# Optimization experiments

Measured on AMD Instinct MI355X. Metric: run time of the kernel, lower is better.

Reference implementation:

```python
import jax, jax.numpy as jnp
import numpy as np
import math

B, L, D, H = 4, 2048, 1024, 16
HD = D // H


def setup_inputs() -> dict:
    key = jax.random.key(0)
    k1, k2, k3 = jax.random.split(key, 3)
    x = jax.random.normal(k1, (B, L, D), dtype=jnp.float32)
    # Linear weights stored as [in, out] so y = x @ W (equivalent to torch x @ W.T)
    Wqkv = jax.random.normal(k2, (D, 3 * D), dtype=jnp.float32) * (1.0 / math.sqrt(D))
    Wproj = jax.random.normal(k3, (D, D), dtype=jnp.float32) * (1.0 / math.sqrt(D))
    attn_mask = jnp.tril(jnp.ones((L, L), dtype=bool))  # True = attend (causal)
    key_padding_mask = jnp.zeros((B, L), dtype=bool)     # True = padded (none here)
    return {"x": x, "Wqkv": Wqkv, "Wproj": Wproj,
            "attn_mask": attn_mask, "key_padding_mask": key_padding_mask}


def reference(x, Wqkv, Wproj, attn_mask, key_padding_mask):
    Bx, Lx, Dx = x.shape
    qkv = x @ Wqkv                              # [B, L, 3D]
    q, k, v = jnp.split(qkv, 3, axis=-1)
    def shape(t):
        return t.reshape(Bx, Lx, H, HD).transpose(0, 2, 1, 3)  # [B, H, L, hd]
    q, k, v = shape(q), shape(k), shape(v)
    att = jnp.einsum('bhqd,bhkd->bhqk', q, k) / math.sqrt(HD)  # [B, H, L, L]
    neg_inf = jnp.float32(-jnp.inf)
    att = jnp.where(attn_mask[None, None, :, :], att, neg_inf)
    att = jnp.where(key_padding_mask[:, None, None, :], neg_inf, att)
    att = jax.nn.softmax(att, axis=-1)
    y = jnp.einsum('bhqk,bhkd->bhqd', att, v)   # [B, H, L, hd]
    y = y.transpose(0, 2, 1, 3).reshape(Bx, Lx, Dx)
    return y @ Wproj
```

## Files before the change

### kernel.cpp

```cpp
#include <hip/hip_runtime.h>
#include <cstdint>
#include <cstddef>


typedef __attribute__((ext_vector_type(8))) __bf16 bf16x8;
typedef __attribute__((ext_vector_type(4))) __bf16 bf16x4;
typedef __attribute__((ext_vector_type(4))) float f32x4;

__device__ __forceinline__ f32x4 mfma_bf16(bf16x8 a, bf16x8 b, f32x4 c) {
  return __builtin_amdgcn_mfma_f32_16x16x32_bf16(a, b, c, 0, 0, 0);
}

__device__ __forceinline__ void async_copy16(const void* gsrc, void* ldsdst) {
  __builtin_amdgcn_global_load_lds(
      (const __attribute__((address_space(1))) void*)gsrc,
      (__attribute__((address_space(3))) void*)ldsdst, 16, 0, 0);
}

__global__ __launch_bounds__(256) void f32_to_bf16(
    const float* __restrict__ in, __bf16* __restrict__ out) {
  const size_t i = ((size_t)blockIdx.x * 256 + threadIdx.x) * 4;
  const float4 v = *(const float4*)&in[i];
  bf16x4 o = {(__bf16)v.x, (__bf16)v.y, (__bf16)v.z, (__bf16)v.w};
  *(bf16x4*)&out[i] = o;
}

__global__ __launch_bounds__(256) void transpose_f32_bf16(
    const float* __restrict__ in, __bf16* __restrict__ out, int R, int C) {
  __shared__ float tile[32][33];
  const int c0 = blockIdx.x * 32;
  const int r0 = blockIdx.y * 32;
  const int tx = threadIdx.x & 31;
  const int ty = threadIdx.x >> 5;
#pragma unroll
  for (int i = 0; i < 32; i += 8)
    tile[ty + i][tx] = in[(size_t)(r0 + ty + i) * C + c0 + tx];
  __syncthreads();
#pragma unroll
  for (int i = 0; i < 32; i += 8)
    out[(size_t)(c0 + ty + i) * R + r0 + tx] = (__bf16)tile[tx][ty + i];
}


__global__ __launch_bounds__(256) void gemm_bt_f32out(
    const __bf16* __restrict__ A, const __bf16* __restrict__ BT,
    float* __restrict__ C, int M, int N, int K) {
  __shared__ __bf16 As[128 * 32];
  __shared__ __bf16 Bs[128 * 32];
  const int tid = threadIdx.x;
  const int wave = tid >> 6;
  const int lane = tid & 63;
  const int n16 = lane & 15;
  const int quad = lane >> 4;
  const int m0 = blockIdx.x * 128;
  const int n0 = blockIdx.y * 128;
  const int wr = wave >> 1;
  const int wc = wave & 1;

  const f32x4 zero = {0.f, 0.f, 0.f, 0.f};
  f32x4 acc[4][4];
#pragma unroll
  for (int i = 0; i < 4; ++i)
#pragma unroll
    for (int j = 0; j < 4; ++j) acc[i][j] = zero;

  const int KT = K >> 5;
  for (int kt = 0; kt < KT; ++kt) {
    const int k0 = kt << 5;
#pragma unroll
    for (int r = 0; r < 2; ++r) {
      const int li = (r << 8) + tid;
      const int row = li >> 2;
      const int kp8 = (li & 3) << 3;
      const int lbase = ((r << 8) + (wave << 6)) << 3;
      async_copy16(&A[(size_t)(m0 + row) * K + k0 + kp8], &As[lbase]);
      async_copy16(&BT[(size_t)(n0 + row) * K + k0 + kp8], &Bs[lbase]);
    }
    __syncthreads();
    bf16x8 af[4], bf[4];
#pragma unroll
    for (int t = 0; t < 4; ++t) {
      af[t] = *(const bf16x8*)&As[(wr * 64 + t * 16 + n16) * 32 + quad * 8];
      bf[t] = *(const bf16x8*)&Bs[(wc * 64 + t * 16 + n16) * 32 + quad * 8];
    }
#pragma unroll
    for (int mt = 0; mt < 4; ++mt)
#pragma unroll
      for (int nt = 0; nt < 4; ++nt)
        acc[mt][nt] = mfma_bf16(af[mt], bf[nt], acc[mt][nt]);
    __syncthreads();
  }
#pragma unroll
  for (int mt = 0; mt < 4; ++mt) {
#pragma unroll
    for (int r = 0; r < 4; ++r) {
      const int m = m0 + wr * 64 + mt * 16 + quad * 4 + r;
#pragma unroll
      for (int nt = 0; nt < 4; ++nt) {
        const int n = n0 + wc * 64 + nt * 16 + n16;
        C[(size_t)m * N + n] = acc[mt][nt][r];
      }
    }
  }
}

__global__ __launch_bounds__(256) void gemm_qkv(
    const __bf16* __restrict__ A, const __bf16* __restrict__ BT,
    __bf16* __restrict__ Q, __bf16* __restrict__ Kh, __bf16* __restrict__ VT) {
  __shared__ __bf16 As[128 * 32];
  __shared__ __bf16 Bs[128 * 32];
  const int tid = threadIdx.x;
  const int wave = tid >> 6;
  const int lane = tid & 63;
  const int n16 = lane & 15;
  const int quad = lane >> 4;
  const int m0 = blockIdx.x * 128;
  const int n0 = blockIdx.y * 128;
  const int wr = wave >> 1;
  const int wc = wave & 1;
  const int K = 1024;

  const f32x4 zero = {0.f, 0.f, 0.f, 0.f};
  f32x4 acc[4][4];
#pragma unroll
  for (int i = 0; i < 4; ++i)
#pragma unroll
    for (int j = 0; j < 4; ++j) acc[i][j] = zero;

  for (int kt = 0; kt < 32; ++kt) {
    const int k0 = kt << 5;
#pragma unroll
    for (int r = 0; r < 2; ++r) {
      const int li = (r << 8) + tid;
      const int row = li >> 2;
      const int kp8 = (li & 3) << 3;
      const int lbase = ((r << 8) + (wave << 6)) << 3;
      async_copy16(&A[(size_t)(m0 + row) * K + k0 + kp8], &As[lbase]);
      async_copy16(&BT[(size_t)(n0 + row) * K + k0 + kp8], &Bs[lbase]);
    }
    __syncthreads();
    bf16x8 af[4], bf[4];
#pragma unroll
    for (int t = 0; t < 4; ++t) {
      af[t] = *(const bf16x8*)&As[(wr * 64 + t * 16 + n16) * 32 + quad * 8];
      bf[t] = *(const bf16x8*)&Bs[(wc * 64 + t * 16 + n16) * 32 + quad * 8];
    }
#pragma unroll
    for (int mt = 0; mt < 4; ++mt)
#pragma unroll
      for (int nt = 0; nt < 4; ++nt)
        acc[mt][nt] = mfma_bf16(af[mt], bf[nt], acc[mt][nt]);
    __syncthreads();
  }

  __syncthreads();
  const int b = m0 >> 11;
  __bf16* tw = (wave < 2 ? As : Bs) + (wave & 1) * 2048;
  const int l0w = (m0 & 2047) + wr * 64;

  if (n0 < 2048) {
    const float QSCALE = 0.125f * 1.44269504089f;
    const bool isQ = (n0 < 1024);
    const int h = ((n0 & 1023) >> 6) + wc;
    __bf16* dst = isQ ? Q : Kh;
    const size_t base = ((size_t)(b * 16 + h) * 2048) * 64;
#pragma unroll
    for (int pass = 0; pass < 2; ++pass) {
#pragma unroll
      for (int mt = 2 * pass; mt < 2 * pass + 2; ++mt) {
#pragma unroll
        for (int nt = 0; nt < 4; ++nt)
#pragma unroll
          for (int r = 0; r < 4; ++r) {
            const int hd = nt * 16 + n16;
            const int mm = (mt & 1) * 16 + quad * 4 + r;
            const float v =
                isQ ? acc[mt][nt][r] * QSCALE : acc[mt][nt][r];
            tw[mm * 64 + (((hd >> 3) ^ (mm & 7)) << 3) + (hd & 7)] =
                (__bf16)v;
          }
      }
#pragma unroll
      for (int i = 0; i < 4; ++i) {
        const int c = lane + 64 * i;
        const int row = c >> 3;
        const int hd0 = (c & 7) << 3;
        const int phys = (c & 7) ^ (row & 7);
        const bf16x8 v = *(const bf16x8*)&tw[row * 64 + phys * 8];
        *(bf16x8*)&dst[base + (size_t)(l0w + pass * 32 + row) * 64 + hd0] = v;
      }
    }
  } else {
    const int h = ((n0 - 2048) >> 6) + wc;
    const size_t bhead = (size_t)(b * 16 + h);
#pragma unroll
    for (int pass = 0; pass < 2; ++pass) {
#pragma unroll
      for (int nt = 2 * pass; nt < 2 * pass + 2; ++nt) {
#pragma unroll
        for (int mt = 0; mt < 4; ++mt)
#pragma unroll
          for (int r = 0; r < 4; ++r) {
            const int hdp = (nt & 1) * 16 + n16;
            const int mm = mt * 16 + quad * 4 + r;
            const int phys = (mm >> 3) ^ (hdp & 7);
            tw[hdp * 64 + phys * 8 + (mm & 7)] = (__bf16)acc[mt][nt][r];
          }
      }
#pragma unroll
      for (int i = 0; i < 4; ++i) {
        const int c = lane + 64 * i;
        const int row = c >> 3;
        const int phys = (c & 7) ^ (row & 7);
        const bf16x8 v = *(const bf16x8*)&tw[row * 64 + phys * 8];
        *(bf16x8*)&VT[(bhead * 64 + pass * 32 + row) * 2048 + l0w +
                      (c & 7) * 8] = v;
      }
    }
  }
}

__global__ __launch_bounds__(256, 4) void flash_attn(
    const __bf16* __restrict__ Q, const __bf16* __restrict__ Kh,
    const __bf16* __restrict__ VT, __bf16* __restrict__ Y) {
  __shared__ __bf16 KsB[2][32 * 64];
  __shared__ __bf16 VsB[2][64 * 32];
  __shared__ __bf16 Ps[4][16 * 40];
  const int bh = blockIdx.x;
  const int p = blockIdx.y;
  const int tid = threadIdx.x;
  const int wave = tid >> 6;
  const int lane = tid & 63;
  const int n16 = lane & 15;
  const int quad = lane >> 4;
  __bf16* pb = Ps[wave];
  const __bf16* Qb = Q + (size_t)bh * 2048 * 64;
  const __bf16* Kb = Kh + (size_t)bh * 2048 * 64;
  const __bf16* Vb = VT + (size_t)bh * 64 * 2048;
  const int b = bh >> 4;
  const int h = bh & 15;
  const f32x4 zero = {0.f, 0.f, 0.f, 0.f};

  const int krow = wave * 8 + (lane >> 3);
  const int kcol8 = (((lane & 7) ^ (lane >> 3)) << 3);
  const int vrow = wave * 16 + (lane >> 2);
  const int vcol8 = (((lane & 3) ^ quad) << 3);

#pragma unroll
  for (int t = 0; t < 2; ++t) {
    const int qt = t == 0 ? p : 31 - p;
    const int q0w = qt * 64 + wave * 16;

    bf16x8 qf[2];
#pragma unroll
    for (int kh = 0; kh < 2; ++kh)
      qf[kh] = *(const bf16x8*)&Qb[(size_t)(q0w + n16) * 64 + kh * 32 +
                                   quad * 8];

    f32x4 o[4];
#pragma unroll
    for (int j = 0; j < 4; ++j) o[j] = zero;
    float lsum = 0.f;

    const int nsteps = 2 * qt + 2;

    async_copy16(&Kb[(size_t)krow * 64 + kcol8], &KsB[0][wave * 512]);
    async_copy16(&Vb[(size_t)vrow * 2048 + vcol8], &VsB[0][wave * 512]);

    for (int kt = 0; kt < nsteps; ++kt) {
      const int buf = kt & 1;
      const int c0 = kt * 32;
      __syncthreads();
      if (kt + 1 < nsteps) {
        const int nb = buf ^ 1;
        const int cn = c0 + 32;
        async_copy16(&Kb[(size_t)(cn + krow) * 64 + kcol8],
                     &KsB[nb][wave * 512]);
        async_copy16(&Vb[(size_t)vrow * 2048 + cn + vcol8],
                     &VsB[nb][wave * 512]);
      }
      const __bf16* ks = KsB[buf];
      const __bf16* vs = VsB[buf];

      f32x4 s[2];
      s[0] = zero;
      s[1] = zero;
#pragma unroll
      for (int ct = 0; ct < 2; ++ct) {
#pragma unroll
        for (int kh = 0; kh < 2; ++kh) {
          const bf16x8 kf = *(const bf16x8*)&ks[(ct * 16 + n16) * 64 +
                                                (((kh * 4 + quad) ^ (n16 & 7))
                                                 << 3)];
          s[ct] = mfma_bf16(kf, qf[kh], s[ct]);
        }
      }
      if (kt >= 2 * qt) {
        const int myq = q0w + n16;
#pragma unroll
        for (int ct = 0; ct < 2; ++ct)
#pragma unroll
          for (int r = 0; r < 4; ++r) {
            const int kcol = c0 + ct * 16 + quad * 4 + r;
            float e = __builtin_amdgcn_exp2f(s[ct][r]);
            e = (kcol <= myq) ? e : 0.f;
            s[ct][r] = e;
            lsum += e;
          }
      } else {
#pragma unroll
        for (int ct = 0; ct < 2; ++ct)
#pragma unroll
          for (int r = 0; r < 4; ++r) {
            const float e = __builtin_amdgcn_exp2f(s[ct][r]);
            s[ct][r] = e;
            lsum += e;
          }
      }
#pragma unroll
      for (int ct = 0; ct < 2; ++ct) {
        const bf16x4 pk = {(__bf16)s[ct][0], (__bf16)s[ct][1],
                           (__bf16)s[ct][2], (__bf16)s[ct][3]};
        *(bf16x4*)&pb[n16 * 40 + ct * 16 + quad * 4] = pk;
      }
      const bf16x8 pa = *(const bf16x8*)&pb[n16 * 40 + quad * 8];
#pragma unroll
      for (int ht = 0; ht < 4; ++ht) {
        const bf16x8 vf = *(const bf16x8*)&vs[(ht * 16 + n16) * 32 +
                                              ((quad ^ (n16 >> 2)) << 3)];
        o[ht] = mfma_bf16(pa, vf, o[ht]);
      }
    }

    lsum += __shfl_xor(lsum, 16);
    lsum += __shfl_xor(lsum, 32);
    const float inv = 1.0f / lsum;
#pragma unroll
    for (int r = 0; r < 4; ++r) {
      const float invr = __shfl(inv, quad * 4 + r);
      const int row = q0w + quad * 4 + r;
#pragma unroll
      for (int ht = 0; ht < 4; ++ht)
        Y[(size_t)(b * 2048 + row) * 1024 + h * 64 + ht * 16 + n16] =
            (__bf16)(o[ht][r] * invr);
    }
  }
}

extern "C" void kernel_launch(void* const* d_in, const int* in_sizes, int n_in,
                              void* d_out, int out_size, void* d_ws,
                              size_t ws_size, hipStream_t stream) {
  const float* x = (const float*)d_in[0];
  const float* Wqkv = (const float*)d_in[1];
  const float* Wproj = (const float*)d_in[2];
  float* out = (float*)d_out;

  char* ws = (char*)d_ws;
  __bf16* xb = (__bf16*)ws;     ws += (size_t)8192 * 1024 * 2;
  __bf16* WqkvT = (__bf16*)ws;  ws += (size_t)3072 * 1024 * 2;
  __bf16* WprojT = (__bf16*)ws; ws += (size_t)1024 * 1024 * 2;
  __bf16* Qs = (__bf16*)ws;     ws += (size_t)64 * 2048 * 64 * 2;
  __bf16* Ks = (__bf16*)ws;     ws += (size_t)64 * 2048 * 64 * 2;
  __bf16* VTs = (__bf16*)ws;    ws += (size_t)64 * 64 * 2048 * 2;
  __bf16* attn = xb;

  f32_to_bf16<<<8192, 256, 0, stream>>>(x, xb);
  transpose_f32_bf16<<<dim3(96, 32), 256, 0, stream>>>(Wqkv, WqkvT, 1024, 3072);
  transpose_f32_bf16<<<dim3(32, 32), 256, 0, stream>>>(Wproj, WprojT, 1024, 1024);
  gemm_qkv<<<dim3(64, 24), 256, 0, stream>>>(xb, WqkvT, Qs, Ks, VTs);
  flash_attn<<<dim3(64, 16), 256, 0, stream>>>(Qs, Ks, VTs, attn);
  gemm_bt_f32out<<<dim3(64, 8), 256, 0, stream>>>(attn, WprojT, out,
                                                  8192, 1024, 1024);
}
```

Baseline: 262.2 us.

## Rework flash attention on 32x32 MFMA with register-resident P via permlane swap

Flash attention now uses 32x32x16 bf16 MFMA tiles. Each wave owns 32 query rows and each block processes 128-query tiles against 64-key tiles, with a paired light/heavy tile schedule. The softmax probabilities go to the PV MFMA through packed bf16 conversion and v_permlane32_swap instead of an LDS round trip, and waves skip key tiles wholly above their causal diagonal. The grid is halved and launch bounds are relaxed to 2 blocks per CU to allow more registers. The costs are lower occupancy, idle waves during skipped steps, and scattered scalar stores on output.

```diff
diff --git a/kernel.cpp b/kernel.cpp
--- a/kernel.cpp
+++ b/kernel.cpp
@@ -6,9 +6,20 @@
 typedef __attribute__((ext_vector_type(8))) __bf16 bf16x8;
 typedef __attribute__((ext_vector_type(4))) __bf16 bf16x4;
 typedef __attribute__((ext_vector_type(4))) float f32x4;
+typedef __attribute__((ext_vector_type(16))) float f32x16;
 
 __device__ __forceinline__ f32x4 mfma_bf16(bf16x8 a, bf16x8 b, f32x4 c) {
   return __builtin_amdgcn_mfma_f32_16x16x32_bf16(a, b, c, 0, 0, 0);
+}
+
+__device__ __forceinline__ f32x16 mfma32(bf16x8 a, bf16x8 b, f32x16 c) {
+  return __builtin_amdgcn_mfma_f32_32x32x16_bf16(a, b, c, 0, 0, 0);
+}
+
+__device__ __forceinline__ unsigned cvtpk(float a, float b) {
+  unsigned r;
+  asm("v_cvt_pk_bf16_f32 %0, %1, %2" : "=v"(r) : "v"(a), "v"(b));
+  return r;
 }
 
 __device__ __forceinline__ void async_copy16(const void* gsrc, void* ldsdst) {
@@ -220,129 +231,149 @@
   }
 }
 
-__global__ __launch_bounds__(256, 4) void flash_attn(
+__global__ __launch_bounds__(256, 2) void flash_attn(
     const __bf16* __restrict__ Q, const __bf16* __restrict__ Kh,
     const __bf16* __restrict__ VT, __bf16* __restrict__ Y) {
-  __shared__ __bf16 KsB[2][32 * 64];
-  __shared__ __bf16 VsB[2][64 * 32];
-  __shared__ __bf16 Ps[4][16 * 40];
+  __shared__ __bf16 Ks[2][64 * 64];
+  __shared__ __bf16 Vs[2][64 * 64];
   const int bh = blockIdx.x;
   const int p = blockIdx.y;
   const int tid = threadIdx.x;
   const int wave = tid >> 6;
   const int lane = tid & 63;
-  const int n16 = lane & 15;
-  const int quad = lane >> 4;
-  __bf16* pb = Ps[wave];
+  const int lrow = lane & 31;
+  const int hi = lane >> 5;
+  const int lswz = lane & 7;
   const __bf16* Qb = Q + (size_t)bh * 2048 * 64;
   const __bf16* Kb = Kh + (size_t)bh * 2048 * 64;
   const __bf16* Vb = VT + (size_t)bh * 64 * 2048;
   const int b = bh >> 4;
   const int h = bh & 15;
-  const f32x4 zero = {0.f, 0.f, 0.f, 0.f};
-
-  const int krow = wave * 8 + (lane >> 3);
-  const int kcol8 = (((lane & 7) ^ (lane >> 3)) << 3);
-  const int vrow = wave * 16 + (lane >> 2);
-  const int vcol8 = (((lane & 3) ^ quad) << 3);
-
-#pragma unroll
-  for (int t = 0; t < 2; ++t) {
-    const int qt = t == 0 ? p : 31 - p;
-    const int q0w = qt * 64 + wave * 16;
-
-    bf16x8 qf[2];
-#pragma unroll
-    for (int kh = 0; kh < 2; ++kh)
-      qf[kh] = *(const bf16x8*)&Qb[(size_t)(q0w + n16) * 64 + kh * 32 +
-                                   quad * 8];
-
-    f32x4 o[4];
-#pragma unroll
-    for (int j = 0; j < 4; ++j) o[j] = zero;
+  const f32x16 zero16 = {0.f, 0.f, 0.f, 0.f, 0.f, 0.f, 0.f, 0.f,
+                         0.f, 0.f, 0.f, 0.f, 0.f, 0.f, 0.f, 0.f};
+
+  const int srow = tid >> 3;
+  const int sswz = ((tid & 7) ^ (srow & 7)) << 3;
+  const size_t kg0 = (size_t)srow * 64 + sswz;
+  const size_t kg1 = (size_t)(srow + 32) * 64 + sswz;
+  const size_t vg0 = (size_t)srow * 2048 + sswz;
+  const size_t vg1 = (size_t)(srow + 32) * 2048 + sswz;
+  const int ldst0 = wave * 512;
+  const int ldst1 = 2048 + wave * 512;
+
+#pragma unroll
+  for (int tt = 0; tt < 2; ++tt) {
+    const int t = tt ? 15 - p : p;
+    const int q0w = t * 128 + wave * 32;
+    const int myq = q0w + lrow;
+
+    bf16x8 qf[4];
+#pragma unroll
+    for (int i = 0; i < 4; ++i)
+      qf[i] = *(const bf16x8*)&Qb[(size_t)myq * 64 + i * 16 + hi * 8];
+
+    f32x16 o0 = zero16, o1 = zero16;
     float lsum = 0.f;
-
-    const int nsteps = 2 * qt + 2;
-
-    async_copy16(&Kb[(size_t)krow * 64 + kcol8], &KsB[0][wave * 512]);
-    async_copy16(&Vb[(size_t)vrow * 2048 + vcol8], &VsB[0][wave * 512]);
+    const int nsteps = 2 * (t + 1);
+
+    __syncthreads();
+    async_copy16(&Kb[kg0], &Ks[0][ldst0]);
+    async_copy16(&Kb[kg1], &Ks[0][ldst1]);
+    async_copy16(&Vb[vg0], &Vs[0][ldst0]);
+    async_copy16(&Vb[vg1], &Vs[0][ldst1]);
 
     for (int kt = 0; kt < nsteps; ++kt) {
       const int buf = kt & 1;
-      const int c0 = kt * 32;
+      const int c0 = kt << 6;
       __syncthreads();
       if (kt + 1 < nsteps) {
         const int nb = buf ^ 1;
-        const int cn = c0 + 32;
-        async_copy16(&Kb[(size_t)(cn + krow) * 64 + kcol8],
-                     &KsB[nb][wave * 512]);
-        async_copy16(&Vb[(size_t)vrow * 2048 + cn + vcol8],
-                     &VsB[nb][wave * 512]);
-      }
-      const __bf16* ks = KsB[buf];
-      const __bf16* vs = VsB[buf];
-
-      f32x4 s[2];
-      s[0] = zero;
-      s[1] = zero;
-#pragma unroll
-      for (int ct = 0; ct < 2; ++ct) {
-#pragma unroll
-        for (int kh = 0; kh < 2; ++kh) {
-          const bf16x8 kf = *(const bf16x8*)&ks[(ct * 16 + n16) * 64 +
-                                                (((kh * 4 + quad) ^ (n16 & 7))
-                                                 << 3)];
-          s[ct] = mfma_bf16(kf, qf[kh], s[ct]);
+        const int cn = c0 + 64;
+        async_copy16(&Kb[kg0 + (size_t)cn * 64], &Ks[nb][ldst0]);
+        async_copy16(&Kb[kg1 + (size_t)cn * 64], &Ks[nb][ldst1]);
+        async_copy16(&Vb[vg0 + cn], &Vs[nb][ldst0]);
+        async_copy16(&Vb[vg1 + cn], &Vs[nb][ldst1]);
+      }
+      if (c0 > q0w + 31) continue;
+
+      const __bf16* ks = Ks[buf];
+      const __bf16* vs = Vs[buf];
+
+      f32x16 sc[2];
+#pragma unroll
+      for (int ch = 0; ch < 2; ++ch) {
+        sc[ch] = zero16;
+#pragma unroll
+        for (int i = 0; i < 4; ++i) {
+          const bf16x8 kf = *(const bf16x8*)&ks[(ch * 32 + lrow) * 64 +
+                                                (((2 * i + hi) ^ lswz) << 3)];
+          sc[ch] = mfma32(kf, qf[i], sc[ch]);
         }
       }
-      if (kt >= 2 * qt) {
-        const int myq = q0w + n16;
-#pragma unroll
-        for (int ct = 0; ct < 2; ++ct)
-#pragma unroll
-          for (int r = 0; r < 4; ++r) {
-            const int kcol = c0 + ct * 16 + quad * 4 + r;
-            float e = __builtin_amdgcn_exp2f(s[ct][r]);
-            e = (kcol <= myq) ? e : 0.f;
-            s[ct][r] = e;
+      if (c0 + 63 > q0w) {
+#pragma unroll
+        for (int ch = 0; ch < 2; ++ch)
+#pragma unroll
+          for (int r = 0; r < 16; ++r) {
+            const int k = c0 + ch * 32 + (r & 3) + 8 * (r >> 2) + 4 * hi;
+            float e = __builtin_amdgcn_exp2f(sc[ch][r]);
+            e = (k <= myq) ? e : 0.f;
+            sc[ch][r] = e;
             lsum += e;
           }
       } else {
 #pragma unroll
-        for (int ct = 0; ct < 2; ++ct)
-#pragma unroll
-          for (int r = 0; r < 4; ++r) {
-            const float e = __builtin_amdgcn_exp2f(s[ct][r]);
-            s[ct][r] = e;
+        for (int ch = 0; ch < 2; ++ch)
+#pragma unroll
+          for (int r = 0; r < 16; ++r) {
+            const float e = __builtin_amdgcn_exp2f(sc[ch][r]);
+            sc[ch][r] = e;
             lsum += e;
           }
       }
 #pragma unroll
-      for (int ct = 0; ct < 2; ++ct) {
-        const bf16x4 pk = {(__bf16)s[ct][0], (__bf16)s[ct][1],
-                           (__bf16)s[ct][2], (__bf16)s[ct][3]};
-        *(bf16x4*)&pb[n16 * 40 + ct * 16 + quad * 4] = pk;
-      }
-      const bf16x8 pa = *(const bf16x8*)&pb[n16 * 40 + quad * 8];
-#pragma unroll
-      for (int ht = 0; ht < 4; ++ht) {
-        const bf16x8 vf = *(const bf16x8*)&vs[(ht * 16 + n16) * 32 +
-                                              ((quad ^ (n16 >> 2)) << 3)];
-        o[ht] = mfma_bf16(pa, vf, o[ht]);
-      }
-    }
-
-    lsum += __shfl_xor(lsum, 16);
+      for (int ch = 0; ch < 2; ++ch) {
+#pragma unroll
+        for (int kc = 0; kc < 2; ++kc) {
+          unsigned c01 = cvtpk(sc[ch][kc * 8 + 0], sc[ch][kc * 8 + 1]);
+          unsigned c23 = cvtpk(sc[ch][kc * 8 + 2], sc[ch][kc * 8 + 3]);
+          unsigned c45 = cvtpk(sc[ch][kc * 8 + 4], sc[ch][kc * 8 + 5]);
+          unsigned c67 = cvtpk(sc[ch][kc * 8 + 6], sc[ch][kc * 8 + 7]);
+          asm("v_permlane32_swap_b32 %0, %1" : "+v"(c01), "+v"(c45));
+          asm("v_permlane32_swap_b32 %0, %1" : "+v"(c23), "+v"(c67));
+          union {
+            unsigned u[4];
+            bf16x8 v;
+          } pu;
+          pu.u[0] = c01;
+          pu.u[1] = c23;
+          pu.u[2] = c45;
+          pu.u[3] = c67;
+          const int kch = ch * 4 + kc * 2 + hi;
+          {
+            const bf16x8 vf0 = *(const bf16x8*)&vs[(0 * 32 + lrow) * 64 +
+                                                   ((kch ^ lswz) << 3)];
+            o0 = mfma32(pu.v, vf0, o0);
+            const bf16x8 vf1 = *(const bf16x8*)&vs[(1 * 32 + lrow) * 64 +
+                                                   ((kch ^ lswz) << 3)];
+            o1 = mfma32(pu.v, vf1, o1);
+          }
+        }
+      }
+    }
+
     lsum += __shfl_xor(lsum, 32);
     const float inv = 1.0f / lsum;
-#pragma unroll
-    for (int r = 0; r < 4; ++r) {
-      const float invr = __shfl(inv, quad * 4 + r);
-      const int row = q0w + quad * 4 + r;
-#pragma unroll
-      for (int ht = 0; ht < 4; ++ht)
-        Y[(size_t)(b * 2048 + row) * 1024 + h * 64 + ht * 16 + n16] =
-            (__bf16)(o[ht][r] * invr);
+    float invr[16];
+#pragma unroll
+    for (int r = 0; r < 16; ++r)
+      invr[r] = __shfl(inv, (r & 3) + 8 * (r >> 2) + 4 * hi);
+#pragma unroll
+    for (int r = 0; r < 16; ++r) {
+      const int row = q0w + (r & 3) + 8 * (r >> 2) + 4 * hi;
+      const size_t yb = (size_t)(b * 2048 + row) * 1024 + h * 64;
+      Y[yb + lrow] = (__bf16)(o0[r] * invr[r]);
+      Y[yb + 32 + lrow] = (__bf16)(o1[r] * invr[r]);
     }
   }
 }
@@ -368,7 +399,7 @@
   transpose_f32_bf16<<<dim3(96, 32), 256, 0, stream>>>(Wqkv, WqkvT, 1024, 3072);
   transpose_f32_bf16<<<dim3(32, 32), 256, 0, stream>>>(Wproj, WprojT, 1024, 1024);
   gemm_qkv<<<dim3(64, 24), 256, 0, stream>>>(xb, WqkvT, Qs, Ks, VTs);
-  flash_attn<<<dim3(64, 16), 256, 0, stream>>>(Qs, Ks, VTs, attn);
+  flash_attn<<<dim3(64, 8), 256, 0, stream>>>(Qs, Ks, VTs, attn);
   gemm_bt_f32out<<<dim3(64, 8), 256, 0, stream>>>(attn, WprojT, out,
                                                   8192, 1024, 1024);
 }
```

Measured after the change: 247.0 us. -5.8%, faster.
